# Optimization experiments

Measured on AMD Instinct MI355X. Metric: run time of the kernel, lower is better.

Reference implementation:

```python
import jax, jax.numpy as jnp
import numpy as np
from jax import lax

B, N, C, H = 16, 577, 1024, 16
D = C // H          # head_dim = 64
M = 24              # spatial side, M*M = N-1
CH = C // 4         # conv bottleneck channels = 256
EPS = 1e-5


def _ln(x, g, b):
    mu = jnp.mean(x, axis=-1, keepdims=True)
    var = jnp.mean((x - mu) ** 2, axis=-1, keepdims=True)
    return (x - mu) * lax.rsqrt(var + EPS) * g + b


def setup_inputs() -> dict:
    key = jax.random.key(0)
    ks = jax.random.split(key, 8)
    s = 0.02
    return {
        "x": jax.random.normal(ks[0], (B, N, C), jnp.float32),
        "ln1_g": jnp.ones((C,), jnp.float32),
        "ln1_b": jnp.zeros((C,), jnp.float32),
        "in_w": jax.random.normal(ks[1], (3 * C, C), jnp.float32) * s,
        "in_b": jnp.zeros((3 * C,), jnp.float32),
        "out_w": jax.random.normal(ks[2], (C, C), jnp.float32) * s,
        "out_b": jnp.zeros((C,), jnp.float32),
        "ln2_g": jnp.ones((C,), jnp.float32),
        "ln2_b": jnp.zeros((C,), jnp.float32),
        "conv1_w": jax.random.normal(ks[3], (CH, C, 3, 3), jnp.float32) * s,
        "conv1_b": jnp.zeros((CH,), jnp.float32),
        "conv2_w": jax.random.normal(ks[4], (C, CH, 3, 3), jnp.float32) * s,
        "conv2_b": jnp.zeros((C,), jnp.float32),
    }


def reference(x, ln1_g, ln1_b, in_w, in_b, out_w, out_b, ln2_g, ln2_b,
              conv1_w, conv1_b, conv2_w, conv2_b):
    residual = x
    h = _ln(x, ln1_g, ln1_b)
    # qkv projection: (B,N,3C) -> (3,B,H,N,D)
    qkv = (h @ in_w.T + in_b).reshape(B, N, 3, H, D).transpose(2, 0, 3, 1, 4)
    q, k, v = qkv[0], qkv[1], qkv[2]
    scale = D ** (-0.5)
    scores = jnp.einsum("bhnd,bhmd->bhnm", q, k) * scale   # (B,H,N,N)
    attn = jax.nn.softmax(scores, axis=-1)
    o = jnp.einsum("bhnm,bhmd->bhnd", attn, v)
    o = o.transpose(0, 2, 1, 3).reshape(B, N, C)
    o = o @ out_w.T + out_b
    x = o + residual                                       # first residual

    y = _ln(x, ln2_g, ln2_b)
    f = y[:, :-1, :].reshape(B, M, M, C).transpose(0, 3, 1, 2)   # NCHW
    c = y[:, -1:, :]                                             # class token
    f = lax.conv_general_dilated(f, conv1_w, (1, 1), "SAME",
                                 dimension_numbers=("NCHW", "OIHW", "NCHW"))
    f = jax.nn.gelu(f + conv1_b[None, :, None, None])
    f = lax.conv_general_dilated(f, conv2_w, (1, 1), "SAME",
                                 dimension_numbers=("NCHW", "OIHW", "NCHW"))
    f = f + conv2_b[None, :, None, None]
    f = f.transpose(0, 2, 3, 1).reshape(B, N - 1, C)
    y = jnp.concatenate((f, c), axis=1)
    return x + y
```

## Files before the change

kernel.cpp:

```cpp
#include <hip/hip_runtime.h>

typedef unsigned short u16;
typedef unsigned int u32;
typedef __bf16 bf16x8 __attribute__((ext_vector_type(8)));
typedef float f32x4 __attribute__((ext_vector_type(4)));

#define DEVI __device__ __forceinline__

#define BB 16
#define NN 577
#define CC 1024
#define HH 16
#define DD 64
#define BN 9232
#define PIX 576
#define WW 24
#define CHN 256
#define VROW 584
#define PSZ (9216 * 256)

DEVI u16 f2b(float f) {
  u32 u = __builtin_bit_cast(u32, f);
  u32 r = 0x7FFFu + ((u >> 16) & 1u);
  return (u16)((u + r) >> 16);
}

DEVI float b2f(u16 h) { return __builtin_bit_cast(float, (u32)h << 16); }

DEVI bf16x8 ldfrag(const u16* p) {
  uint4 u = *(const uint4*)p;
  return __builtin_bit_cast(bf16x8, u);
}

DEVI f32x4 mfma16(bf16x8 a, bf16x8 b, f32x4 c) {
  return __builtin_amdgcn_mfma_f32_16x16x32_bf16(a, b, c, 0, 0, 0);
}

DEVI void gld_lds16(const u16* g, u16* l) {
  __builtin_amdgcn_global_load_lds((const __attribute__((address_space(1))) void*)g,
                                   (__attribute__((address_space(3))) void*)l, 16, 0, 0);
}

DEVI float gelu_tanh(float v) {
  const float x3 = v * v * v;
  const float t = __expf(1.5957691216057308f * (v + 0.044715f * x3));
  const float th = (t - 1.f) / (t + 1.f);
  return 0.5f * v * (1.f + th);
}

__global__ __launch_bounds__(256) void prep_kernel(
    const float* __restrict__ in_w, const float* __restrict__ out_w,
    const float* __restrict__ c1w, const float* __restrict__ c2w,
    u16* __restrict__ wqkv, u16* __restrict__ wout,
    u16* __restrict__ w1t, u16* __restrict__ w2t, u16* __restrict__ zpad) {
  const int i0 = blockIdx.x * 256 + threadIdx.x;
  const int stride = gridDim.x * 256;
  for (int i = i0; i < 3072 * 1024; i += stride) wqkv[i] = f2b(in_w[i]);
  for (int i = i0; i < 1024 * 1024; i += stride) wout[i] = f2b(out_w[i]);
  for (int i = i0; i < 256 * 9216; i += stride) {
    int oc = i / 9216, rem = i - oc * 9216, tap = rem >> 10, c = rem & 1023;
    w1t[i] = f2b(c1w[(size_t)oc * 9216 + c * 9 + tap]);
  }
  for (int i = i0; i < 1024 * 2304; i += stride) {
    int oc = i / 2304, rem = i - oc * 2304, tap = rem >> 8, c = rem & 255;
    w2t[i] = f2b(c2w[(size_t)oc * 2304 + c * 9 + tap]);
  }
  if (i0 < 128) zpad[i0] = 0;
}

template <int MODE>
__global__ __launch_bounds__(256) void ln_kernel(
    const float* __restrict__ xin, const float* __restrict__ gam,
    const float* __restrict__ bet, u16* __restrict__ yout, float* __restrict__ oextra) {
  __shared__ float sh[8];
  const int row = blockIdx.x;
  const int tid = threadIdx.x;
  const float4 v = ((const float4*)(xin + (size_t)row * CC))[tid];
  float s = v.x + v.y + v.z + v.w;
  float qq = v.x * v.x + v.y * v.y + v.z * v.z + v.w * v.w;
#pragma unroll
  for (int off = 32; off > 0; off >>= 1) {
    s += __shfl_down(s, off);
    qq += __shfl_down(qq, off);
  }
  if ((tid & 63) == 0) { sh[tid >> 6] = s; sh[4 + (tid >> 6)] = qq; }
  __syncthreads();
  s = sh[0] + sh[1] + sh[2] + sh[3];
  qq = sh[4] + sh[5] + sh[6] + sh[7];
  const float mu = s * (1.f / 1024.f);
  const float rstd = rsqrtf(qq * (1.f / 1024.f) - mu * mu + 1e-5f);
  const float4 g4 = ((const float4*)gam)[tid];
  const float4 b4 = ((const float4*)bet)[tid];
  const float o0 = (v.x - mu) * rstd * g4.x + b4.x;
  const float o1 = (v.y - mu) * rstd * g4.y + b4.y;
  const float o2 = (v.z - mu) * rstd * g4.z + b4.z;
  const float o3 = (v.w - mu) * rstd * g4.w + b4.w;
  ushort4 st = make_ushort4(f2b(o0), f2b(o1), f2b(o2), f2b(o3));
  *(ushort4*)(yout + (size_t)row * CC + tid * 4) = st;
  if constexpr (MODE == 1) {
    if (row % NN == NN - 1) {
      float4 ov = make_float4(v.x + o0, v.y + o1, v.z + o2, v.w + o3);
      ((float4*)(oextra + (size_t)row * CC))[tid] = ov;
    }
  }
}

struct GArgs {
  const u16* A; const u16* Bm; const float* bias; const float* res;
  float* outF; u16* outH; u16* outQ; u16* outK; u16* outV; const u16* zpad;
  int M, K;
};

template <int MODE>
__global__ __launch_bounds__(256) void gemm_kernel(GArgs ag) {
  __shared__ u16 SH[24576];
  const int tid = threadIdx.x;
  const int w = tid >> 6, l = tid & 63;
  const int wr = w >> 1, wc = w & 1;
  const int lr = l & 15, lg = l >> 4;
  const int bid = blockIdx.x;
  int mt, nt, tapz = 0;
  if constexpr (MODE == 0) {
    const int g = (bid & 7) * 219 + (bid >> 3);
    nt = g / 73; mt = g - nt * 73;
  } else if constexpr (MODE == 1) {
    nt = bid & 7; mt = bid >> 3;
  } else if constexpr (MODE == 3) {
    nt = bid & 7; mt = bid >> 3;
  } else {
    const int g = (bid & 7) * 162 + (bid >> 3);
    tapz = g / 144;
    const int rem = g - tapz * 144;
    nt = rem / 72; mt = rem - nt * 72;
  }
  const int m0 = mt * 128, n0 = nt * 128;
  const int rA = w * 16 + (l >> 2);
  const int cbs = ((l & 3) ^ ((l >> 3) & 3)) * 8;

  auto stage = [&](int buf, int kt) {
    const int k0 = kt * 32;
    u16* Ald = SH + buf * 4096;
    u16* Bld = SH + 12288 + buf * 4096;
#pragma unroll
    for (int c = 0; c < 2; ++c) {
      const int r = c * 64 + rA;
      const u16* asrc;
      if constexpr (MODE <= 1) {
        int m = m0 + r;
        m = m < ag.M ? m : ag.M - 1;
        asrc = ag.A + (size_t)m * ag.K + (k0 + cbs);
      } else {
        const int m = m0 + r;
        const int b = m / PIX, p = m - b * PIX;
        const int py = p / WW, px = p - py * WW;
        constexpr int CKc = (MODE == 3) ? 256 : 1024;
        const int tap = (MODE == 4) ? tapz : (k0 / CKc);
        const int c0 = (MODE == 4) ? k0 : (k0 - tap * CKc);
        const int py2 = py + (tap / 3) - 1, px2 = px + (tap % 3) - 1;
        if ((u32)py2 < (u32)WW && (u32)px2 < (u32)WW) {
          if constexpr (MODE == 4)
            asrc = ag.A + ((size_t)(b * NN + py2 * WW + px2) * CC + c0 + cbs);
          else
            asrc = ag.A + ((size_t)(b * PIX + py2 * WW + px2) * CHN + c0 + cbs);
        } else {
          asrc = ag.zpad + cbs;
        }
      }
      gld_lds16(asrc, &Ald[c * 2048 + w * 512]);
      const u16* bsrc;
      if constexpr (MODE == 4)
        bsrc = ag.Bm + (size_t)(n0 + r) * 9216 + (tapz * 1024 + k0 + cbs);
      else
        bsrc = ag.Bm + (size_t)(n0 + r) * ag.K + (k0 + cbs);
      gld_lds16(bsrc, &Bld[c * 2048 + w * 512]);
    }
  };

  f32x4 acc[4][4] = {};
  const int KL = (MODE == 4) ? 1024 : ag.K;
  const int nst = KL >> 5;

  stage(0, 0);
  stage(1, 1);

  const int swz = (lr >> 1) & 3;
  int b0 = 0, b1 = 1, b2 = 2;
  for (int kt = 0; kt < nst; ++kt) {
    if (kt + 1 < nst) { asm volatile("s_waitcnt vmcnt(4)" ::: "memory"); }
    else              { asm volatile("s_waitcnt vmcnt(0)" ::: "memory"); }
    __builtin_amdgcn_s_barrier();
    if (kt + 2 < nst) stage(b2, kt + 2);
    bf16x8 af[4], bfr[4];
#pragma unroll
    for (int i = 0; i < 4; ++i)
      af[i] = ldfrag(&SH[b0 * 4096 + (wr * 64 + i * 16 + lr) * 32 + ((lg ^ swz) * 8)]);
#pragma unroll
    for (int i = 0; i < 4; ++i)
      bfr[i] = ldfrag(&SH[12288 + b0 * 4096 + (wc * 64 + i * 16 + lr) * 32 + ((lg ^ swz) * 8)]);
    __builtin_amdgcn_s_setprio(1);
#pragma unroll
    for (int mi = 0; mi < 4; ++mi)
#pragma unroll
      for (int ni = 0; ni < 4; ++ni) acc[mi][ni] = mfma16(af[mi], bfr[ni], acc[mi][ni]);
    __builtin_amdgcn_s_setprio(0);
    const int tmp = b0; b0 = b1; b1 = b2; b2 = tmp;
  }

  if constexpr (MODE == 0) {
    if (n0 >= 2048) {
      __syncthreads();
      const int G0 = m0 + wr * 64;
      const int b0q = G0 / NN;
      const bool ok = (G0 + 63 < ag.M) && (b0q == (G0 + 63) / NN);
      const int h = (n0 + wc * 64 - 2048) >> 6;
      u16* scr = SH + w * 5120;
      if (ok) {
#pragma unroll
        for (int mi = 0; mi < 4; ++mi) {
#pragma unroll
          for (int ni = 0; ni < 4; ++ni) {
            ushort4 st;
            const float bv = ag.bias[n0 + wc * 64 + ni * 16 + lr];
            st.x = f2b(acc[mi][ni][0] + bv);
            st.y = f2b(acc[mi][ni][1] + bv);
            st.z = f2b(acc[mi][ni][2] + bv);
            st.w = f2b(acc[mi][ni][3] + bv);
            *(ushort4*)(scr + (ni * 16 + lr) * 80 + mi * 16 + lg * 4) = st;
          }
        }
        asm volatile("s_waitcnt lgkmcnt(0)" ::: "memory");
        const int nb = G0 - b0q * NN;
        u16* vb = ag.outV + (size_t)((b0q * 16 + h) * 64) * VROW;
#pragma unroll
        for (int pass = 0; pass < 8; ++pass) {
          const int d_ = pass * 8 + (l >> 3);
          const int nn = (l & 7) * 8;
          uint4 vv = *(const uint4*)(scr + d_ * 80 + nn);
          u16* dst = vb + (size_t)d_ * VROW + nb + nn;
          if (!(nb & 1)) {
            ((u32*)dst)[0] = vv.x; ((u32*)dst)[1] = vv.y;
            ((u32*)dst)[2] = vv.z; ((u32*)dst)[3] = vv.w;
          } else {
            u16 tmp[8];
            *(uint4*)tmp = vv;
#pragma unroll
            for (int j = 0; j < 8; ++j) dst[j] = tmp[j];
          }
        }
      } else {
#pragma unroll
        for (int mi = 0; mi < 4; ++mi) {
#pragma unroll
          for (int r = 0; r < 4; ++r) {
            const int row = G0 + mi * 16 + lg * 4 + r;
            if (row >= ag.M) continue;
            const int b = row / NN, n = row - b * NN;
#pragma unroll
            for (int ni = 0; ni < 4; ++ni) {
              const int col = n0 + wc * 64 + ni * 16 + lr;
              const int d = col & 63;
              const float v = acc[mi][ni][r] + ag.bias[col];
              ag.outV[((size_t)((b * 16 + h) * 64 + d)) * VROW + n] = f2b(v);
            }
          }
        }
      }
      return;
    }
#pragma unroll
    for (int mi = 0; mi < 4; ++mi) {
#pragma unroll
      for (int r = 0; r < 4; ++r) {
        const int row = m0 + wr * 64 + mi * 16 + lg * 4 + r;
        if (row >= ag.M) continue;
        const int b = row / NN, n = row - b * NN;
#pragma unroll
        for (int ni = 0; ni < 4; ++ni) {
          const int col = n0 + wc * 64 + ni * 16 + lr;
          const int which = col >> 10, hd = col & 1023, h = hd >> 6, d = hd & 63;
          const float v = acc[mi][ni][r] + ag.bias[col];
          if (which == 0)
            ag.outQ[((size_t)(b * 16 + h) * NN + n) * DD + d] = f2b(v * 0.18033688011112042f);
          else
            ag.outK[((size_t)(b * 16 + h) * NN + n) * DD + d] = f2b(v);
        }
      }
    }
  } else {
#pragma unroll
    for (int mi = 0; mi < 4; ++mi) {
#pragma unroll
      for (int r = 0; r < 4; ++r) {
        const int row = m0 + wr * 64 + mi * 16 + lg * 4 + r;
        if (row >= ag.M) continue;
#pragma unroll
        for (int ni = 0; ni < 4; ++ni) {
          const int col = n0 + wc * 64 + ni * 16 + lr;
          if constexpr (MODE == 4) {
            u16* pb = (tapz < 5) ? ag.outH : ag.outQ;
            const int tl = (tapz < 5) ? tapz : tapz - 5;
            pb[(size_t)tl * PSZ + (size_t)row * CHN + col] = f2b(acc[mi][ni][r]);
          } else {
            const float v = acc[mi][ni][r] + ag.bias[col];
            if constexpr (MODE == 1) {
              const size_t idx = (size_t)row * CC + col;
              ag.outF[idx] = v + ag.res[idx];
            } else {
              const int b = row / PIX, p = row - b * PIX;
              const size_t idx = (size_t)(b * NN + p) * CC + col;
              ag.outF[idx] = v + ag.res[idx];
            }
          }
        }
      }
    }
  }
}

__global__ __launch_bounds__(256) void gelu_reduce_kernel(
    const u16* __restrict__ pA, const u16* __restrict__ pB,
    const float* __restrict__ bias, u16* __restrict__ f1) {
  const size_t i4 = ((size_t)blockIdx.x * 256 + threadIdx.x) * 4;
  const int col = (int)(i4 & 255);
  float s0 = 0.f, s1 = 0.f, s2 = 0.f, s3 = 0.f;
#pragma unroll
  for (int t = 0; t < 5; ++t) {
    ushort4 u = *(const ushort4*)(pA + (size_t)t * PSZ + i4);
    s0 += b2f(u.x); s1 += b2f(u.y); s2 += b2f(u.z); s3 += b2f(u.w);
  }
#pragma unroll
  for (int t = 0; t < 4; ++t) {
    ushort4 u = *(const ushort4*)(pB + (size_t)t * PSZ + i4);
    s0 += b2f(u.x); s1 += b2f(u.y); s2 += b2f(u.z); s3 += b2f(u.w);
  }
  const float4 b4 = *(const float4*)(bias + col);
  ushort4 st = make_ushort4(f2b(gelu_tanh(s0 + b4.x)), f2b(gelu_tanh(s1 + b4.y)),
                            f2b(gelu_tanh(s2 + b4.z)), f2b(gelu_tanh(s3 + b4.w)));
  *(ushort4*)(f1 + i4) = st;
}

__global__ __launch_bounds__(512) void attn_kernel(
    const u16* __restrict__ q, const u16* __restrict__ k,
    const u16* __restrict__ vt, u16* __restrict__ o) {
  __shared__ u16 SH2[24576];
  const int tid = threadIdx.x;
  const int w = tid >> 6, l = tid & 63;
  const int lr = l & 15, lg = l >> 4;
  const int lg4 = lg * 4;
  const int bid = blockIdx.x;
  const int xcd = bid & 7, gg = bid >> 3;
  const int bh = (gg / 5) * 8 + xcd;
  const int qt = gg % 5;
  const int b = bh >> 4, h = bh & 15;

  const u16* qp = q + (size_t)bh * NN * DD;
  const u16* kp = k + (size_t)bh * NN * DD;
  const u16* vp = vt + (size_t)bh * DD * VROW;

  const int qrow = qt * 128 + w * 16 + lr;
  const int qrc = qrow < NN ? qrow : NN - 1;
  const bf16x8 qf0 = ldfrag(qp + (size_t)qrc * DD + lg * 8);
  const bf16x8 qf1 = ldfrag(qp + (size_t)qrc * DD + 32 + lg * 8);

  const int srow = l >> 3;
  const int schk = (l & 7) ^ (srow & 7);
  auto stage = [&](int buf, int kt) {
    const int kb = kt * 64;
    gld_lds16(kp + (size_t)(kb + w * 8 + srow) * DD + schk * 8,
              &SH2[buf * 4096 + w * 512]);
    gld_lds16(vp + (size_t)(w * 8 + srow) * VROW + kb + schk * 8,
              &SH2[8192 + buf * 4096 + w * 512]);
  };

  f32x4 oa[4] = {};
  float mrow = -1e30f;
  float lsum = 0.f;
  u16* pw = &SH2[16384 + w * 1024];
  const int x7 = lr & 7;
  const int x3 = lr & 3;

  stage(0, 0);
  stage(1, 1);

  for (int kt = 0; kt < 10; ++kt) {
    if (kt <= 7) { asm volatile("s_waitcnt vmcnt(2)" ::: "memory"); }
    else         { asm volatile("s_waitcnt vmcnt(0)" ::: "memory"); }
    __builtin_amdgcn_s_barrier();
    const u16* KB = &SH2[(kt & 1) * 4096];
    const u16* VB = &SH2[8192 + (kt & 1) * 4096];
    const int kb = kt * 64;

    f32x4 s[4] = {};
#pragma unroll
    for (int g = 0; g < 4; ++g) {
      const int row = g * 16 + lr;
      const bf16x8 a0 = ldfrag(&KB[row * 64 + ((lg ^ x7) * 8)]);
      const bf16x8 a1 = ldfrag(&KB[row * 64 + (((4 + lg) ^ x7) * 8)]);
      s[g] = mfma16(a0, qf0, s[g]);
      s[g] = mfma16(a1, qf1, s[g]);
    }
    float t[16];
    const bool last = (kt == 9);
#pragma unroll
    for (int g = 0; g < 4; ++g)
#pragma unroll
      for (int r = 0; r < 4; ++r) {
        const int key = kb + g * 16 + lg4 + r;
        t[g * 4 + r] = (!last || key < NN) ? s[g][r] : -3e38f;
      }
    float pmax = t[0];
#pragma unroll
    for (int i = 1; i < 16; ++i) pmax = fmaxf(pmax, t[i]);
    pmax = fmaxf(pmax, __shfl_xor(pmax, 16));
    pmax = fmaxf(pmax, __shfl_xor(pmax, 32));
    if (!__all(pmax <= mrow + 8.f)) {
      const float mn = fmaxf(mrow, pmax);
      const float corr = exp2f(mrow - mn);
      mrow = mn;
      lsum *= corr;
      float bc[4];
#pragma unroll
      for (int r = 0; r < 4; ++r) bc[r] = __shfl(corr, (l & 48) | (lg4 + r));
#pragma unroll
      for (int g = 0; g < 4; ++g)
#pragma unroll
        for (int r = 0; r < 4; ++r) oa[g][r] *= bc[r];
    }
    float ps[16];
    float rsum = 0.f;
#pragma unroll
    for (int i = 0; i < 16; ++i) { ps[i] = exp2f(t[i] - mrow); rsum += ps[i]; }
    rsum += __shfl_xor(rsum, 16);
    rsum += __shfl_xor(rsum, 32);
    lsum += rsum;
#pragma unroll
    for (int g = 0; g < 4; ++g) {
      u32 w0, w1;
      asm("v_cvt_pk_bf16_f32 %0, %1, %2" : "=v"(w0) : "v"(ps[g * 4 + 0]), "v"(ps[g * 4 + 1]));
      asm("v_cvt_pk_bf16_f32 %0, %1, %2" : "=v"(w1) : "v"(ps[g * 4 + 2]), "v"(ps[g * 4 + 3]));
      const int lc = (g & 1) * 2 + (lg >> 1);
      const int off = (g >> 1) * 512 + lr * 32 + ((lc ^ x3) * 8) + (lg & 1) * 4;
      *(uint2*)(&pw[off]) = make_uint2(w0, w1);
    }
    asm volatile("s_waitcnt lgkmcnt(0)" ::: "memory");
    const bf16x8 paf = ldfrag(&pw[lr * 32 + ((lg ^ x3) * 8)]);
    const bf16x8 pbf = ldfrag(&pw[512 + lr * 32 + ((lg ^ x3) * 8)]);
#pragma unroll
    for (int dg = 0; dg < 4; ++dg) {
      const int row = dg * 16 + lr;
      const bf16x8 v0 = ldfrag(&VB[row * 64 + ((lg ^ x7) * 8)]);
      const bf16x8 v1 = ldfrag(&VB[row * 64 + (((4 + lg) ^ x7) * 8)]);
      oa[dg] = mfma16(paf, v0, oa[dg]);
      oa[dg] = mfma16(pbf, v1, oa[dg]);
    }
    asm volatile("s_waitcnt lgkmcnt(0)" ::: "memory");
    __builtin_amdgcn_s_barrier();
    if (kt + 2 <= 9) stage(kt & 1, kt + 2);
  }

  const int nq = qt * 128 + w * 16 + lg4;
  float linv[4];
#pragma unroll
  for (int r = 0; r < 4; ++r) linv[r] = __shfl(lsum, (l & 48) | (lg4 + r));
#pragma unroll
  for (int r = 0; r < 4; ++r) {
    const int n = nq + r;
    if (n >= NN) continue;
    const float inv = 1.0f / linv[r];
#pragma unroll
    for (int g = 0; g < 4; ++g)
      o[(size_t)(b * NN + n) * CC + h * DD + g * 16 + lr] = f2b(oa[g][r] * inv);
  }
}

extern "C" void kernel_launch(void* const* d_in, const int* in_sizes, int n_in,
                              void* d_out, int out_size, void* d_ws, size_t ws_size,
                              hipStream_t stream) {
  const float* x     = (const float*)d_in[0];
  const float* ln1_g = (const float*)d_in[1];
  const float* ln1_b = (const float*)d_in[2];
  const float* in_w  = (const float*)d_in[3];
  const float* in_b  = (const float*)d_in[4];
  const float* out_w = (const float*)d_in[5];
  const float* out_b = (const float*)d_in[6];
  const float* ln2_g = (const float*)d_in[7];
  const float* ln2_b = (const float*)d_in[8];
  const float* c1w   = (const float*)d_in[9];
  const float* c1b   = (const float*)d_in[10];
  const float* c2w   = (const float*)d_in[11];
  const float* c2b   = (const float*)d_in[12];
  float* out = (float*)d_out;

  char* ws = (char*)d_ws;
  size_t off = 0;
  auto alloc = [&](size_t bytes) {
    void* p = ws + off;
    off += (bytes + 255) & ~(size_t)255;
    return p;
  };
  u16* hb   = (u16*)alloc((size_t)BN * CC * 2);
  u16* wqkv = (u16*)alloc((size_t)3072 * 1024 * 2);
  u16* wout = (u16*)alloc((size_t)1024 * 1024 * 2);
  u16* w1t  = (u16*)alloc((size_t)256 * 9216 * 2);
  u16* w2t  = (u16*)alloc((size_t)1024 * 2304 * 2);
  u16* qb   = (u16*)alloc((size_t)256 * NN * DD * 2);
  u16* kb   = (u16*)alloc((size_t)256 * NN * DD * 2);
  u16* vtb  = (u16*)alloc((size_t)256 * DD * VROW * 2 + 16384);
  float* x2 = (float*)alloc((size_t)BN * CC * 4);
  u16* zpad = (u16*)alloc(256);
  u16* ob = hb;
  u16* yb = qb;
  u16* f1 = kb;
  u16* pA = hb;
  u16* pB = vtb;

  prep_kernel<<<1024, 256, 0, stream>>>(in_w, out_w, c1w, c2w, wqkv, wout, w1t, w2t, zpad);
  ln_kernel<0><<<BN, 256, 0, stream>>>(x, ln1_g, ln1_b, hb, nullptr);
  {
    GArgs a{hb, wqkv, in_b, nullptr, nullptr, nullptr, qb, kb, vtb, zpad, BN, CC};
    gemm_kernel<0><<<1752, 256, 0, stream>>>(a);
  }
  attn_kernel<<<1280, 512, 0, stream>>>(qb, kb, vtb, ob);
  {
    GArgs a{ob, wout, out_b, x, x2, nullptr, nullptr, nullptr, nullptr, zpad, BN, CC};
    gemm_kernel<1><<<584, 256, 0, stream>>>(a);
  }
  ln_kernel<1><<<BN, 256, 0, stream>>>(x2, ln2_g, ln2_b, yb, out);
  {
    GArgs a{yb, w1t, c1b, nullptr, nullptr, pA, pB, nullptr, nullptr, zpad, 9216, 9216};
    gemm_kernel<4><<<1296, 256, 0, stream>>>(a);
  }
  gelu_reduce_kernel<<<2304, 256, 0, stream>>>(pA, pB, c1b, f1);
  {
    GArgs a{f1, w2t, c2b, x2, out, nullptr, nullptr, nullptr, nullptr, zpad, 9216, 2304};
    gemm_kernel<3><<<576, 256, 0, stream>>>(a);
  }
}
```

Baseline: 408.4 us.

## Add dedicated 256x256-tile QKV GEMM kernel and store residual stream in bf16

Replaces the generic 128x128 QKV projection GEMM with a dedicated 512-thread kernel that computes 256x256 tiles. It uses a 64-wide K step, double-buffered direct-to-LDS loads with XOR swizzling, and an XCD-aware tile mapping. Separately, the first residual output x2 is now stored as bf16 instead of fp32, halving traffic for the out-projection store, the LN2 read, and the final residual read. The bf16 residual lowers precision on the skip path, and the large-tile kernel runs at one block per CU with a fixed tile-count mapping.

Result: faster. 380.2 us, median of 2 (-6.9%).

```diff
diff --git a/kernel.cpp b/kernel.cpp
--- a/kernel.cpp
+++ b/kernel.cpp
@@ -70,12 +70,19 @@
 
 template <int MODE>
 __global__ __launch_bounds__(256) void ln_kernel(
-    const float* __restrict__ xin, const float* __restrict__ gam,
-    const float* __restrict__ bet, u16* __restrict__ yout, float* __restrict__ oextra) {
+    const float* __restrict__ xf, const u16* __restrict__ xh,
+    const float* __restrict__ gam, const float* __restrict__ bet,
+    u16* __restrict__ yout, float* __restrict__ oextra) {
   __shared__ float sh[8];
   const int row = blockIdx.x;
   const int tid = threadIdx.x;
-  const float4 v = ((const float4*)(xin + (size_t)row * CC))[tid];
+  float4 v;
+  if constexpr (MODE == 0) {
+    v = ((const float4*)(xf + (size_t)row * CC))[tid];
+  } else {
+    ushort4 uv = ((const ushort4*)(xh + (size_t)row * CC))[tid];
+    v = make_float4(b2f(uv.x), b2f(uv.y), b2f(uv.z), b2f(uv.w));
+  }
   float s = v.x + v.y + v.z + v.w;
   float qq = v.x * v.x + v.y * v.y + v.z * v.z + v.w * v.w;
 #pragma unroll
@@ -106,10 +113,173 @@
 }
 
 struct GArgs {
-  const u16* A; const u16* Bm; const float* bias; const float* res;
+  const u16* A; const u16* Bm; const float* bias; const float* res; const u16* resH;
   float* outF; u16* outH; u16* outQ; u16* outK; u16* outV; const u16* zpad;
   int M, K;
 };
+
+__global__ __launch_bounds__(512, 1) void qkv_kernel(GArgs ag) {
+  __shared__ u16 SH[65536];
+  const int tid = threadIdx.x;
+  const int w = tid >> 6, l = tid & 63;
+  const int wm = w >> 2, wn = w & 3;
+  const int lr = l & 15, lg = l >> 4;
+  const int orig = blockIdx.x;
+  const int xcd = orig & 7;
+  const int wg = (xcd < 4 ? xcd * 56 : 224 + (xcd - 4) * 55) + (orig >> 3);
+  const int nt = wg / 37, mt = wg - nt * 37;
+  const int m0 = mt * 256, n0 = nt * 256;
+
+  const int srow = tid >> 3;
+  const int schk = tid & 7;
+
+  auto stageA = [&](int buf, int kt, int j) {
+    const int row = j * 64 + srow;
+    const int ch = schk ^ (row & 7);
+    int m = m0 + row;
+    m = m < ag.M ? m : ag.M - 1;
+    gld_lds16(ag.A + (size_t)m * 1024 + kt * 64 + ch * 8,
+              &SH[buf * 16384 + (j * 64 + w * 8) * 64]);
+  };
+  auto stageB = [&](int buf, int kt, int j) {
+    const int row = j * 64 + srow;
+    const int ch = schk ^ (row & 7);
+    gld_lds16(ag.Bm + (size_t)(n0 + row) * 1024 + kt * 64 + ch * 8,
+              &SH[32768 + buf * 16384 + (j * 64 + w * 8) * 64]);
+  };
+
+  f32x4 acc[8][4] = {};
+
+#pragma unroll
+  for (int j = 0; j < 4; ++j) { stageA(0, 0, j); stageB(0, 0, j); }
+
+  for (int kt = 0; kt < 16; ++kt) {
+    asm volatile("s_waitcnt vmcnt(0)" ::: "memory");
+    __builtin_amdgcn_s_barrier();
+    const int bf = kt & 1, nb = bf ^ 1;
+    const u16* AB = &SH[bf * 16384];
+    const u16* BBm = &SH[32768 + bf * 16384];
+    bf16x8 bfr[4];
+#pragma unroll
+    for (int ph = 0; ph < 4; ++ph) {
+      const int mg = (ph & 1) << 2;
+      const int kh = ph >> 1;
+      bf16x8 af[4];
+#pragma unroll
+      for (int i = 0; i < 4; ++i) {
+        const int ra = wm * 128 + (mg + i) * 16 + lr;
+        af[i] = ldfrag(&AB[ra * 64 + (((kh << 2) + lg) ^ (ra & 7)) * 8]);
+      }
+      if ((ph & 1) == 0) {
+#pragma unroll
+        for (int i = 0; i < 4; ++i) {
+          const int rb = wn * 64 + i * 16 + lr;
+          bfr[i] = ldfrag(&BBm[rb * 64 + (((kh << 2) + lg) ^ (rb & 7)) * 8]);
+        }
+      }
+      if (kt + 1 < 16) {
+        stageA(nb, kt + 1, ph);
+        stageB(nb, kt + 1, ph);
+      }
+      __builtin_amdgcn_s_barrier();
+      asm volatile("s_waitcnt lgkmcnt(0)" ::: "memory");
+      __builtin_amdgcn_s_setprio(1);
+#pragma unroll
+      for (int mi = 0; mi < 4; ++mi)
+#pragma unroll
+        for (int ni = 0; ni < 4; ++ni)
+          acc[mg + mi][ni] = mfma16(af[mi], bfr[ni], acc[mg + mi][ni]);
+      __builtin_amdgcn_s_setprio(0);
+      __builtin_amdgcn_s_barrier();
+    }
+  }
+
+  if (n0 >= 2048) {
+    __syncthreads();
+    const int hh = (n0 + wn * 64 - 2048) >> 6;
+    u16* scr = SH + w * 5120;
+#pragma unroll
+    for (int qh = 0; qh < 2; ++qh) {
+      if (qh) { asm volatile("s_waitcnt lgkmcnt(0)" ::: "memory"); }
+      const int G0 = m0 + wm * 128 + qh * 64;
+      const int b0q = G0 / NN;
+      const bool ok = (G0 + 63 < ag.M) && (b0q == (G0 + 63) / NN);
+      if (ok) {
+#pragma unroll
+        for (int mi = 0; mi < 4; ++mi) {
+#pragma unroll
+          for (int ni = 0; ni < 4; ++ni) {
+            const f32x4 a4 = acc[qh * 4 + mi][ni];
+            const float bv = ag.bias[n0 + wn * 64 + ni * 16 + lr];
+            ushort4 st;
+            st.x = f2b(a4[0] + bv);
+            st.y = f2b(a4[1] + bv);
+            st.z = f2b(a4[2] + bv);
+            st.w = f2b(a4[3] + bv);
+            *(ushort4*)(scr + (ni * 16 + lr) * 80 + mi * 16 + lg * 4) = st;
+          }
+        }
+        asm volatile("s_waitcnt lgkmcnt(0)" ::: "memory");
+        const int nb2 = G0 - b0q * NN;
+        u16* vb = ag.outV + (size_t)((b0q * 16 + hh) * 64) * VROW;
+#pragma unroll
+        for (int pass = 0; pass < 8; ++pass) {
+          const int d_ = pass * 8 + (l >> 3);
+          const int nn = (l & 7) * 8;
+          uint4 vv = *(const uint4*)(scr + d_ * 80 + nn);
+          u16* dst = vb + (size_t)d_ * VROW + nb2 + nn;
+          if (!(nb2 & 1)) {
+            ((u32*)dst)[0] = vv.x; ((u32*)dst)[1] = vv.y;
+            ((u32*)dst)[2] = vv.z; ((u32*)dst)[3] = vv.w;
+          } else {
+            u16 tmp[8];
+            *(uint4*)tmp = vv;
+#pragma unroll
+            for (int j = 0; j < 8; ++j) dst[j] = tmp[j];
+          }
+        }
+      } else {
+#pragma unroll
+        for (int mi = 0; mi < 4; ++mi) {
+#pragma unroll
+          for (int r = 0; r < 4; ++r) {
+            const int row = G0 + mi * 16 + lg * 4 + r;
+            if (row >= ag.M) continue;
+            const int b = row / NN, n = row - b * NN;
+#pragma unroll
+            for (int ni = 0; ni < 4; ++ni) {
+              const int col = n0 + wn * 64 + ni * 16 + lr;
+              const int d = col & 63;
+              const float v = acc[qh * 4 + mi][ni][r] + ag.bias[col];
+              ag.outV[((size_t)((b * 16 + hh) * 64 + d)) * VROW + n] = f2b(v);
+            }
+          }
+        }
+      }
+    }
+    return;
+  }
+  const bool isQ = n0 < 1024;
+#pragma unroll
+  for (int mi = 0; mi < 8; ++mi) {
+#pragma unroll
+    for (int r = 0; r < 4; ++r) {
+      const int row = m0 + wm * 128 + mi * 16 + (lg << 2) + r;
+      if (row >= ag.M) continue;
+      const int b = row / NN, n = row - b * NN;
+#pragma unroll
+      for (int ni = 0; ni < 4; ++ni) {
+        const int col = n0 + wn * 64 + ni * 16 + lr;
+        const int hd = col & 1023, h = hd >> 6, d = hd & 63;
+        const float v = acc[mi][ni][r] + ag.bias[col];
+        if (isQ)
+          ag.outQ[((size_t)(b * 16 + h) * NN + n) * DD + d] = f2b(v * 0.18033688011112042f);
+        else
+          ag.outK[((size_t)(b * 16 + h) * NN + n) * DD + d] = f2b(v);
+      }
+    }
+  }
+}
 
 template <int MODE>
 __global__ __launch_bounds__(256) void gemm_kernel(GArgs ag) {
@@ -120,12 +290,7 @@
   const int lr = l & 15, lg = l >> 4;
   const int bid = blockIdx.x;
   int mt, nt, tapz = 0;
-  if constexpr (MODE == 0) {
-    const int g = (bid & 7) * 219 + (bid >> 3);
-    nt = g / 73; mt = g - nt * 73;
-  } else if constexpr (MODE == 1) {
-    nt = bid & 7; mt = bid >> 3;
-  } else if constexpr (MODE == 3) {
+  if constexpr (MODE == 1 || MODE == 3) {
     nt = bid & 7; mt = bid >> 3;
   } else {
     const int g = (bid & 7) * 162 + (bid >> 3);
@@ -145,7 +310,7 @@
     for (int c = 0; c < 2; ++c) {
       const int r = c * 64 + rA;
       const u16* asrc;
-      if constexpr (MODE <= 1) {
+      if constexpr (MODE == 1) {
         int m = m0 + r;
         m = m < ag.M ? m : ag.M - 1;
         asrc = ag.A + (size_t)m * ag.K + (k0 + cbs);
@@ -206,111 +371,26 @@
     const int tmp = b0; b0 = b1; b1 = b2; b2 = tmp;
   }
 
-  if constexpr (MODE == 0) {
-    if (n0 >= 2048) {
-      __syncthreads();
-      const int G0 = m0 + wr * 64;
-      const int b0q = G0 / NN;
-      const bool ok = (G0 + 63 < ag.M) && (b0q == (G0 + 63) / NN);
-      const int h = (n0 + wc * 64 - 2048) >> 6;
-      u16* scr = SH + w * 5120;
-      if (ok) {
-#pragma unroll
-        for (int mi = 0; mi < 4; ++mi) {
-#pragma unroll
-          for (int ni = 0; ni < 4; ++ni) {
-            ushort4 st;
-            const float bv = ag.bias[n0 + wc * 64 + ni * 16 + lr];
-            st.x = f2b(acc[mi][ni][0] + bv);
-            st.y = f2b(acc[mi][ni][1] + bv);
-            st.z = f2b(acc[mi][ni][2] + bv);
-            st.w = f2b(acc[mi][ni][3] + bv);
-            *(ushort4*)(scr + (ni * 16 + lr) * 80 + mi * 16 + lg * 4) = st;
-          }
-        }
-        asm volatile("s_waitcnt lgkmcnt(0)" ::: "memory");
-        const int nb = G0 - b0q * NN;
-        u16* vb = ag.outV + (size_t)((b0q * 16 + h) * 64) * VROW;
-#pragma unroll
-        for (int pass = 0; pass < 8; ++pass) {
-          const int d_ = pass * 8 + (l >> 3);
-          const int nn = (l & 7) * 8;
-          uint4 vv = *(const uint4*)(scr + d_ * 80 + nn);
-          u16* dst = vb + (size_t)d_ * VROW + nb + nn;
-          if (!(nb & 1)) {
-            ((u32*)dst)[0] = vv.x; ((u32*)dst)[1] = vv.y;
-            ((u32*)dst)[2] = vv.z; ((u32*)dst)[3] = vv.w;
-          } else {
-            u16 tmp[8];
-            *(uint4*)tmp = vv;
-#pragma unroll
-            for (int j = 0; j < 8; ++j) dst[j] = tmp[j];
-          }
-        }
-      } else {
-#pragma unroll
-        for (int mi = 0; mi < 4; ++mi) {
-#pragma unroll
-          for (int r = 0; r < 4; ++r) {
-            const int row = G0 + mi * 16 + lg * 4 + r;
-            if (row >= ag.M) continue;
-            const int b = row / NN, n = row - b * NN;
-#pragma unroll
-            for (int ni = 0; ni < 4; ++ni) {
-              const int col = n0 + wc * 64 + ni * 16 + lr;
-              const int d = col & 63;
-              const float v = acc[mi][ni][r] + ag.bias[col];
-              ag.outV[((size_t)((b * 16 + h) * 64 + d)) * VROW + n] = f2b(v);
-            }
-          }
-        }
-      }
-      return;
-    }
-#pragma unroll
-    for (int mi = 0; mi < 4; ++mi) {
-#pragma unroll
-      for (int r = 0; r < 4; ++r) {
-        const int row = m0 + wr * 64 + mi * 16 + lg * 4 + r;
-        if (row >= ag.M) continue;
-        const int b = row / NN, n = row - b * NN;
-#pragma unroll
-        for (int ni = 0; ni < 4; ++ni) {
-          const int col = n0 + wc * 64 + ni * 16 + lr;
-          const int which = col >> 10, hd = col & 1023, h = hd >> 6, d = hd & 63;
-          const float v = acc[mi][ni][r] + ag.bias[col];
-          if (which == 0)
-            ag.outQ[((size_t)(b * 16 + h) * NN + n) * DD + d] = f2b(v * 0.18033688011112042f);
-          else
-            ag.outK[((size_t)(b * 16 + h) * NN + n) * DD + d] = f2b(v);
-        }
-      }
-    }
-  } else {
-#pragma unroll
-    for (int mi = 0; mi < 4; ++mi) {
-#pragma unroll
-      for (int r = 0; r < 4; ++r) {
-        const int row = m0 + wr * 64 + mi * 16 + lg * 4 + r;
-        if (row >= ag.M) continue;
-#pragma unroll
-        for (int ni = 0; ni < 4; ++ni) {
-          const int col = n0 + wc * 64 + ni * 16 + lr;
-          if constexpr (MODE == 4) {
-            u16* pb = (tapz < 5) ? ag.outH : ag.outQ;
-            const int tl = (tapz < 5) ? tapz : tapz - 5;
-            pb[(size_t)tl * PSZ + (size_t)row * CHN + col] = f2b(acc[mi][ni][r]);
-          } else {
-            const float v = acc[mi][ni][r] + ag.bias[col];
-            if constexpr (MODE == 1) {
-              const size_t idx = (size_t)row * CC + col;
-              ag.outF[idx] = v + ag.res[idx];
-            } else {
-              const int b = row / PIX, p = row - b * PIX;
-              const size_t idx = (size_t)(b * NN + p) * CC + col;
-              ag.outF[idx] = v + ag.res[idx];
-            }
-          }
+#pragma unroll
+  for (int mi = 0; mi < 4; ++mi) {
+#pragma unroll
+    for (int r = 0; r < 4; ++r) {
+      const int row = m0 + wr * 64 + mi * 16 + lg * 4 + r;
+      if (row >= ag.M) continue;
+#pragma unroll
+      for (int ni = 0; ni < 4; ++ni) {
+        const int col = n0 + wc * 64 + ni * 16 + lr;
+        if constexpr (MODE == 4) {
+          u16* pb = (tapz < 5) ? ag.outH : ag.outQ;
+          const int tl = (tapz < 5) ? tapz : tapz - 5;
+          pb[(size_t)tl * PSZ + (size_t)row * CHN + col] = f2b(acc[mi][ni][r]);
+        } else if constexpr (MODE == 1) {
+          const size_t idx = (size_t)row * CC + col;
+          ag.outH[idx] = f2b(acc[mi][ni][r] + ag.bias[col] + ag.res[idx]);
+        } else {
+          const int b = row / PIX, p = row - b * PIX;
+          const size_t idx = (size_t)(b * NN + p) * CC + col;
+          ag.outF[idx] = acc[mi][ni][r] + ag.bias[col] + b2f(ag.resH[idx]);
         }
       }
     }
@@ -506,7 +586,7 @@
   u16* qb   = (u16*)alloc((size_t)256 * NN * DD * 2);
   u16* kb   = (u16*)alloc((size_t)256 * NN * DD * 2);
   u16* vtb  = (u16*)alloc((size_t)256 * DD * VROW * 2 + 16384);
-  float* x2 = (float*)alloc((size_t)BN * CC * 4);
+  u16* x2h  = (u16*)alloc((size_t)BN * CC * 2);
   u16* zpad = (u16*)alloc(256);
   u16* ob = hb;
   u16* yb = qb;
@@ -515,24 +595,24 @@
   u16* pB = vtb;
 
   prep_kernel<<<1024, 256, 0, stream>>>(in_w, out_w, c1w, c2w, wqkv, wout, w1t, w2t, zpad);
-  ln_kernel<0><<<BN, 256, 0, stream>>>(x, ln1_g, ln1_b, hb, nullptr);
+  ln_kernel<0><<<BN, 256, 0, stream>>>(x, nullptr, ln1_g, ln1_b, hb, nullptr);
   {
-    GArgs a{hb, wqkv, in_b, nullptr, nullptr, nullptr, qb, kb, vtb, zpad, BN, CC};
-    gemm_kernel<0><<<1752, 256, 0, stream>>>(a);
+    GArgs a{hb, wqkv, in_b, nullptr, nullptr, nullptr, nullptr, qb, kb, vtb, zpad, BN, CC};
+    qkv_kernel<<<444, 512, 0, stream>>>(a);
   }
   attn_kernel<<<1280, 512, 0, stream>>>(qb, kb, vtb, ob);
   {
-    GArgs a{ob, wout, out_b, x, x2, nullptr, nullptr, nullptr, nullptr, zpad, BN, CC};
+    GArgs a{ob, wout, out_b, x, nullptr, nullptr, x2h, nullptr, nullptr, nullptr, zpad, BN, CC};
     gemm_kernel<1><<<584, 256, 0, stream>>>(a);
   }
-  ln_kernel<1><<<BN, 256, 0, stream>>>(x2, ln2_g, ln2_b, yb, out);
+  ln_kernel<1><<<BN, 256, 0, stream>>>(nullptr, x2h, ln2_g, ln2_b, yb, out);
   {
-    GArgs a{yb, w1t, c1b, nullptr, nullptr, pA, pB, nullptr, nullptr, zpad, 9216, 9216};
+    GArgs a{yb, w1t, c1b, nullptr, nullptr, nullptr, pA, pB, nullptr, nullptr, zpad, 9216, 9216};
     gemm_kernel<4><<<1296, 256, 0, stream>>>(a);
   }
   gelu_reduce_kernel<<<2304, 256, 0, stream>>>(pA, pB, c1b, f1);
   {
-    GArgs a{f1, w2t, c2b, x2, out, nullptr, nullptr, nullptr, nullptr, zpad, 9216, 2304};
+    GArgs a{f1, w2t, c2b, nullptr, x2h, out, nullptr, nullptr, nullptr, nullptr, zpad, 9216, 2304};
     gemm_kernel<3><<<576, 256, 0, stream>>>(a);
   }
 }
```
